# Performance work log

Measured on AMD Instinct MI355X. Metric: run time of the kernel, lower is better.

The kernel has to match this reference:

```python
import jax, jax.numpy as jnp
import numpy as np

NEG_INF = -1e30

def setup_inputs() -> dict:
    key = jax.random.key(0)
    k1, k2, k3 = jax.random.split(key, 3)
    B, H, S, D = 2, 16, 2048, 128
    q = jax.random.normal(k1, (B, H, S, D), dtype=jnp.float32)
    k = jax.random.normal(k2, (B, H, S, D), dtype=jnp.float32)
    v = jax.random.normal(k3, (B, H, S, D), dtype=jnp.float32)
    return {"q": q, "k": k, "v": v}

def reference(q, k, v):
    # F.scaled_dot_product_attention(q, k, v, is_causal=True), MATH backend:
    # full score matrix, causal mask (top-left aligned: j <= i), softmax, bmm.
    D = q.shape[-1]
    scale = 1.0 / jnp.sqrt(jnp.asarray(D, dtype=q.dtype))
    scores = jnp.einsum('bhqd,bhkd->bhqk', q, k) * scale  # [B,H,S,S]
    Sq, Sk = scores.shape[-2], scores.shape[-1]
    causal = jnp.arange(Sk)[None, :] <= jnp.arange(Sq)[:, None]  # [Sq,Sk]
    scores = jnp.where(causal[None, None], scores, NEG_INF)
    attn = jax.nn.softmax(scores, axis=-1)
    return jnp.einsum('bhqk,bhkd->bhqd', attn, v)
```

## Files before the change

kernel.cpp:

```cpp
#include <hip/hip_runtime.h>
#include <cstdint>
#include <cstddef>

typedef __attribute__((ext_vector_type(8))) short short8;
typedef __attribute__((ext_vector_type(4))) float floatx4;
typedef __attribute__((ext_vector_type(2))) unsigned int uint2v;

namespace {
constexpr int kBH  = 32;
constexpr int kS   = 2048;
constexpr int kD   = 128;
constexpr int kBQ  = 64;
constexpr int kBK  = 32;
constexpr int kNQT = kS / kBQ;
constexpr int PST  = 72;
constexpr size_t kKVElems = (size_t)kBH * kS * kD;
}

__device__ __forceinline__ unsigned short f32_bf16(float f) {
    union { float f; unsigned u; } c; c.f = f;
    unsigned u = c.u;
    u += 0x7FFFu + ((u >> 16) & 1u);
    return (unsigned short)(u >> 16);
}

__device__ __forceinline__ unsigned cvt_pk_bf16(float lo, float hi) {
    unsigned r;
    asm("v_cvt_pk_bf16_f32 %0, %1, %2" : "=v"(r) : "v"(lo), "v"(hi));
    return r;
}

__device__ __forceinline__ unsigned pack_bf16x2(float lo, float hi) {
    return cvt_pk_bf16(lo, hi);
}

__device__ __forceinline__ float fast_exp2(float x) {
#if __has_builtin(__builtin_amdgcn_exp2f)
    return __builtin_amdgcn_exp2f(x);
#else
    return __expf(x * 0.6931471805599453f);
#endif
}

__device__ __forceinline__ void gl_lds16(const void* g, void* l) {
    __builtin_amdgcn_global_load_lds(
        (const __attribute__((address_space(1))) unsigned int*)g,
        (__attribute__((address_space(3))) unsigned int*)l, 16, 0, 0);
}

__global__ __launch_bounds__(256)
void prepass(const float* __restrict__ K, const float* __restrict__ V,
             unsigned short* __restrict__ Kb, unsigned short* __restrict__ Vt) {
    const int b = (int)blockIdx.x;
    const int t = (int)threadIdx.x;
    if (b < 4096) {
        const size_t i0 = ((size_t)b * 256 + t) * 8;
        floatx4 a = *(const floatx4*)(K + i0);
        floatx4 c = *(const floatx4*)(K + i0 + 4);
        union { unsigned u[4]; short8 v; } pk;
        pk.u[0] = cvt_pk_bf16(a[0], a[1]);
        pk.u[1] = cvt_pk_bf16(a[2], a[3]);
        pk.u[2] = cvt_pk_bf16(c[0], c[1]);
        pk.u[3] = cvt_pk_bf16(c[2], c[3]);
        *(short8*)(Kb + i0) = pk.v;
    } else {
        __shared__ float ldsT[64][68];
        const int vb = b - 4096;
        const int bh = vb >> 6;
        const int rem = vb & 63;
        const int s0 = (rem >> 1) * 64;
        const int d0 = (rem & 1) * 64;
        const float* vbase = V + ((size_t)bh * kS + s0) * kD + d0;
        const int sr = t >> 4, c4 = (t & 15) * 4;
#pragma unroll
        for (int p = 0; p < 4; ++p) {
            const int s = p * 16 + sr;
            *(floatx4*)&ldsT[s][c4] = *(const floatx4*)(vbase + (size_t)s * kD + c4);
        }
        __syncthreads();
        const int dr = t >> 2, sc = (t & 3) * 16;
        union { unsigned u[8]; short8 v[2]; } pk;
#pragma unroll
        for (int j = 0; j < 8; ++j)
            pk.u[j] = cvt_pk_bf16(ldsT[sc + 2 * j][dr], ldsT[sc + 2 * j + 1][dr]);
        unsigned short* out = Vt + ((size_t)(bh * kD + d0 + dr)) * kS + s0 + sc;
        *(short8*)out = pk.v[0];
        *(short8*)(out + 8) = pk.v[1];
    }
}


__global__ __launch_bounds__(256, 4)
void fa_fwd_ws(const float* __restrict__ Qg, const unsigned short* __restrict__ Kb,
               const unsigned short* __restrict__ Vt, float* __restrict__ Og) {
    const int id = (int)blockIdx.x;
    const int s  = id >> 8;
    const int j  = id & 255;
    const int bh = (j & 7) * 4 + ((j >> 3) & 3);
    const int a  = j >> 5;
    const int qt = (s == 0) ? a : (s == 1) ? (31 - a) : (s == 2) ? (8 + a) : (23 - a);

    const int t    = (int)threadIdx.x;
    const int wave = t >> 6;
    const int lane = t & 63;
    const int quad = lane >> 4;
    const int l16  = lane & 15;
    const int rowq_base = qt * 64 + wave * 16 + l16;
    const int prm_lo = ((quad & 1) << 7) + (l16 << 2);
    const int prm_hi = prm_lo + 64;
    const bool hi = lane >= 32;

    __shared__ __align__(16) unsigned short kT0[kBK * 128];
    __shared__ __align__(16) unsigned short kT1[kBK * 128];
    __shared__ __align__(16) unsigned short vT0[kD * kBK];
    __shared__ __align__(16) unsigned short vT1[kD * kBK];

    const float scale = 0.12751744459649126f;

    short8  qf[4];
    floatx4 oacc[8];
    float   lsum = 0.f;
#pragma unroll
    for (int i = 0; i < 8; ++i) oacc[i] = (floatx4){0, 0, 0, 0};

    {
        const float* qp = Qg + ((size_t)bh * kS + rowq_base) * kD;
#pragma unroll
        for (int ks = 0; ks < 4; ++ks) {
            const int d0 = ks * 32 + quad * 8;
            floatx4 a0 = *(const floatx4*)(qp + d0);
            floatx4 a1 = *(const floatx4*)(qp + d0 + 4);
            union { unsigned u[4]; short8 v; } pa;
            pa.u[0] = cvt_pk_bf16(a0[0] * scale, a0[1] * scale);
            pa.u[1] = cvt_pk_bf16(a0[2] * scale, a0[3] * scale);
            pa.u[2] = cvt_pk_bf16(a1[0] * scale, a1[1] * scale);
            pa.u[3] = cvt_pk_bf16(a1[2] * scale, a1[3] * scale);
            qf[ks] = pa.v;
        }
    }

    const unsigned short* kBase = Kb + (size_t)bh * kS * kD;
    const unsigned short* vBase = Vt + (size_t)bh * kD * kS;

    auto stage = [&](int kt, unsigned short* kDst, unsigned short* vDst) {
        const int kj0 = kt * kBK;
#pragma unroll
        for (int i = 0; i < 2; ++i) {
            const int rbase = wave * 8 + i * 4;
            const int row = rbase + (lane >> 4);
            const int cg  = (lane & 15) ^ (row & 15);
            gl_lds16(kBase + ((size_t)(kj0 + row)) * kD + cg * 8,
                     &kDst[rbase * 128]);
        }
#pragma unroll
        for (int i = 0; i < 2; ++i) {
            const int dbase = wave * 32 + i * 16;
            const int d  = dbase + (lane >> 2);
            const int cg = (lane & 3) ^ ((d >> 1) & 3);
            gl_lds16(vBase + (size_t)d * kS + kj0 + cg * 8,
                     &vDst[dbase * kBK]);
        }
    };

    auto tile_step = [&](const unsigned short* kT, const unsigned short* vT,
                         bool doMask, int rq) {
        floatx4 sacc[2];
        __builtin_amdgcn_s_setprio(1);
#pragma unroll
        for (int nt = 0; nt < 2; ++nt) {
            floatx4 acc = (floatx4){0.f, 0.f, 0.f, 0.f};
#pragma unroll
            for (int ks = 0; ks < 4; ++ks) {
                short8 kf = *(const short8*)&kT[(nt * 16 + l16) * 128 + (((ks * 4 + quad) ^ l16) << 3)];
                acc = __builtin_amdgcn_mfma_f32_16x16x32_bf16(kf, qf[ks], acc, 0, 0, 0);
            }
            sacc[nt] = acc;
        }
        __builtin_amdgcn_s_setprio(0);

        float ls = 0.f;
#pragma unroll
        for (int nt = 0; nt < 2; ++nt)
#pragma unroll
            for (int r = 0; r < 4; ++r) {
                float e = fast_exp2(sacc[nt][r]);
                if (doMask && (nt * 16 + quad * 4 + r > rq)) e = 0.f;
                sacc[nt][r] = e;
                ls += e;
            }
        lsum += ls;

        unsigned pk0a = cvt_pk_bf16(sacc[0][0], sacc[0][1]);
        unsigned pk0b = cvt_pk_bf16(sacc[0][2], sacc[0][3]);
        unsigned pk1a = cvt_pk_bf16(sacc[1][0], sacc[1][1]);
        unsigned pk1b = cvt_pk_bf16(sacc[1][2], sacc[1][3]);
        int e0 = __builtin_amdgcn_ds_bpermute(prm_lo, (int)pk0a);
        int e1 = __builtin_amdgcn_ds_bpermute(prm_lo, (int)pk0b);
        int e2 = __builtin_amdgcn_ds_bpermute(prm_hi, (int)pk0a);
        int e3 = __builtin_amdgcn_ds_bpermute(prm_hi, (int)pk0b);
        int o0 = __builtin_amdgcn_ds_bpermute(prm_lo, (int)pk1a);
        int o1 = __builtin_amdgcn_ds_bpermute(prm_lo, (int)pk1b);
        int o2 = __builtin_amdgcn_ds_bpermute(prm_hi, (int)pk1a);
        int o3 = __builtin_amdgcn_ds_bpermute(prm_hi, (int)pk1b);
        union { unsigned u[4]; short8 v; } pf;
        pf.u[0] = hi ? (unsigned)o0 : (unsigned)e0;
        pf.u[1] = hi ? (unsigned)o1 : (unsigned)e1;
        pf.u[2] = hi ? (unsigned)o2 : (unsigned)e2;
        pf.u[3] = hi ? (unsigned)o3 : (unsigned)e3;

        __builtin_amdgcn_s_setprio(1);
#pragma unroll
        for (int nd = 0; nd < 8; ++nd) {
            short8 vf = *(const short8*)&vT[(nd * 16 + l16) * kBK + ((quad ^ ((l16 >> 1) & 3)) << 3)];
            oacc[nd] = __builtin_amdgcn_mfma_f32_16x16x32_bf16(pf.v, vf, oacc[nd], 0, 0, 0);
        }
        __builtin_amdgcn_s_setprio(0);
    };

    const int last = 2 * qt + 1;
    stage(0, kT0, vT0);
    __syncthreads();

    int kt = 0;
    for (;;) {
        if (kt < last) stage(kt + 1, kT1, vT1);
        tile_step(kT0, vT0, kt >= 2 * qt, rowq_base - kt * kBK);
        __syncthreads();
        if (kt == last) break;
        ++kt;
        if (kt < last) stage(kt + 1, kT0, vT0);
        tile_step(kT1, vT1, kt >= 2 * qt, rowq_base - kt * kBK);
        __syncthreads();
        if (kt == last) break;
        ++kt;
    }

    float rs = lsum;
    rs += __shfl_xor(rs, 16, 64);
    rs += __shfl_xor(rs, 32, 64);
    float inv[4];
#pragma unroll
    for (int r = 0; r < 4; ++r)
        inv[r] = 1.0f / __shfl(rs, quad * 4 + r, 64);
    float* ob = Og + ((size_t)bh * kS + qt * 64 + wave * 16 + quad * 4) * kD;
#pragma unroll
    for (int nd = 0; nd < 8; ++nd)
#pragma unroll
        for (int r = 0; r < 4; ++r)
            ob[(size_t)r * kD + nd * 16 + l16] = oacc[nd][r] * inv[r];
}

namespace {
constexpr int kBKf = 64;
constexpr int KSTf = 136;
constexpr int VSTf = 72;
}

struct TileStateF {
    short8  qf[4];
    floatx4 oacc[8];
    float   lsum[4];
};

__device__ __forceinline__ void tile_step_f(
    TileStateF& ts, const unsigned short* kT, const unsigned short* vT,
    unsigned short* pw, int l16, int quad, int rowl, bool doMask)
{
    floatx4 sacc[4];
    __builtin_amdgcn_s_setprio(1);
#pragma unroll
    for (int nt = 0; nt < 4; ++nt) {
        floatx4 acc = (floatx4){0.f, 0.f, 0.f, 0.f};
#pragma unroll
        for (int ks = 0; ks < 4; ++ks) {
            short8 kf = *(const short8*)&kT[(nt * 16 + l16) * KSTf + ks * 32 + quad * 8];
            acc = __builtin_amdgcn_mfma_f32_16x16x32_bf16(ts.qf[ks], kf, acc, 0, 0, 0);
        }
        sacc[nt] = acc;
    }
    __builtin_amdgcn_s_setprio(0);
    if (doMask) {
#pragma unroll
        for (int nt = 0; nt < 4; ++nt) {
            const int col = nt * 16 + l16;
#pragma unroll
            for (int r = 0; r < 4; ++r)
                if (col > rowl + r) sacc[nt][r] = -1e30f;
        }
    }
#pragma unroll
    for (int nt = 0; nt < 4; ++nt)
#pragma unroll
        for (int r = 0; r < 4; ++r)
            sacc[nt][r] = fast_exp2(sacc[nt][r]);
#pragma unroll
    for (int r = 0; r < 4; ++r)
        ts.lsum[r] += (sacc[0][r] + sacc[1][r]) + (sacc[2][r] + sacc[3][r]);
#pragma unroll
    for (int r = 0; r < 4; ++r) {
#pragma unroll
        for (int np = 0; np < 2; ++np) {
            const unsigned u = cvt_pk_bf16(sacc[np * 2][r], sacc[np * 2 + 1][r]);
            pw[(quad * 4 + r) * PST + (np * 2) * 16 + l16]     = (unsigned short)u;
            pw[(quad * 4 + r) * PST + (np * 2 + 1) * 16 + l16] = (unsigned short)(u >> 16);
        }
    }
    short8 pf[2];
#pragma unroll
    for (int ks = 0; ks < 2; ++ks)
        pf[ks] = *(const short8*)&pw[l16 * PST + ks * 32 + quad * 8];
    __builtin_amdgcn_s_setprio(1);
#pragma unroll
    for (int nd = 0; nd < 8; ++nd) {
        floatx4 acc = ts.oacc[nd];
#pragma unroll
        for (int ks = 0; ks < 2; ++ks) {
            short8 vf = *(const short8*)&vT[(nd * 16 + l16) * VSTf + ks * 32 + quad * 8];
            acc = __builtin_amdgcn_mfma_f32_16x16x32_bf16(pf[ks], vf, acc, 0, 0, 0);
        }
        ts.oacc[nd] = acc;
    }
    __builtin_amdgcn_s_setprio(0);
}

__global__ __launch_bounds__(256, 2)
void fa_fwd_fallback(const float* __restrict__ Qg, const float* __restrict__ Kg,
                     const float* __restrict__ Vg, float* __restrict__ Og) {
    const int id = (int)blockIdx.x;
    const int qA = id >> 5;
    const int qB = kNQT - 1 - qA;
    const int bh = id & (kBH - 1);
    const int t    = (int)threadIdx.x;
    const int wave = t >> 6;
    const int lane = t & 63;
    const int quad = lane >> 4;
    const int l16  = lane & 15;
    const int rowl = wave * 16 + quad * 4;

    __shared__ __align__(16) unsigned short kT[2][kBKf * KSTf];
    __shared__ __align__(16) unsigned short vT[2][kD * VSTf];
    __shared__ __align__(16) unsigned short pT[4 * 16 * PST];
    unsigned short* pw = &pT[wave * 16 * PST];

    const float scale = 0.12751744459649126f;

    TileStateF A, B;
#pragma unroll
    for (int i = 0; i < 8; ++i) { A.oacc[i] = (floatx4){0,0,0,0}; B.oacc[i] = (floatx4){0,0,0,0}; }
#pragma unroll
    for (int r = 0; r < 4; ++r) { A.lsum[r] = 0.f; B.lsum[r] = 0.f; }
    {
        const float* qpA = Qg + ((size_t)bh * kS + qA * kBQ + wave * 16 + l16) * kD;
        const float* qpB = Qg + ((size_t)bh * kS + qB * kBQ + wave * 16 + l16) * kD;
#pragma unroll
        for (int ks = 0; ks < 4; ++ks) {
            const int d0 = ks * 32 + quad * 8;
            floatx4 a0 = *(const floatx4*)(qpA + d0);
            floatx4 a1 = *(const floatx4*)(qpA + d0 + 4);
            floatx4 b0 = *(const floatx4*)(qpB + d0);
            floatx4 b1 = *(const floatx4*)(qpB + d0 + 4);
            union { unsigned u[4]; short8 v; } pa, pb;
            pa.u[0] = cvt_pk_bf16(a0[0] * scale, a0[1] * scale);
            pa.u[1] = cvt_pk_bf16(a0[2] * scale, a0[3] * scale);
            pa.u[2] = cvt_pk_bf16(a1[0] * scale, a1[1] * scale);
            pa.u[3] = cvt_pk_bf16(a1[2] * scale, a1[3] * scale);
            pb.u[0] = cvt_pk_bf16(b0[0] * scale, b0[1] * scale);
            pb.u[1] = cvt_pk_bf16(b0[2] * scale, b0[3] * scale);
            pb.u[2] = cvt_pk_bf16(b1[0] * scale, b1[1] * scale);
            pb.u[3] = cvt_pk_bf16(b1[2] * scale, b1[3] * scale);
            A.qf[ks] = pa.v;
            B.qf[ks] = pb.v;
        }
    }

    const int kRow8 = t >> 5;
    const int kCol4 = t & 31;
    const int vD    = t & 127;
    const int vR2   = t >> 7;
    const float* kBaseH = Kg + (size_t)bh * kS * kD;
    const float* vBaseH = Vg + (size_t)bh * kS * kD;
    floatx4 kpre[8];
    float   vpreL[16], vpreH[16];

    auto issue_kv_loads = [&](int kt) {
        const float* kb = kBaseH + (size_t)(kt * kBKf) * kD;
        const float* vb = vBaseH + (size_t)(kt * kBKf) * kD;
#pragma unroll
        for (int p = 0; p < 8; ++p)
            kpre[p] = *(const floatx4*)(kb + (size_t)(p * 8 + kRow8) * kD + kCol4 * 4);
#pragma unroll
        for (int p = 0; p < 16; ++p) {
            const int j = p * 2 + vR2;
            vpreL[p] = vb[(size_t)(2 * j) * kD + vD];
            vpreH[p] = vb[(size_t)(2 * j + 1) * kD + vD];
        }
    };
    auto store_kv = [&](int buf) {
#pragma unroll
        for (int p = 0; p < 8; ++p) {
            union { unsigned u[2]; uint2v v; } w;
            w.u[0] = cvt_pk_bf16(kpre[p][0], kpre[p][1]);
            w.u[1] = cvt_pk_bf16(kpre[p][2], kpre[p][3]);
            *(uint2v*)&kT[buf][(p * 8 + kRow8) * KSTf + kCol4 * 4] = w.v;
        }
#pragma unroll
        for (int p = 0; p < 16; ++p) {
            const int j = p * 2 + vR2;
            *(unsigned*)&vT[buf][vD * VSTf + 2 * j] = pack_bf16x2(vpreL[p], vpreH[p]);
        }
    };

    const int last = qB;
    issue_kv_loads(0);
    store_kv(0);
    __syncthreads();
    for (int kt = 0; kt <= last; ++kt) {
        const int buf = kt & 1;
        if (kt < last) issue_kv_loads(kt + 1);
        if (kt <= qA) tile_step_f(A, kT[buf], vT[buf], pw, l16, quad, rowl, kt == qA);
        tile_step_f(B, kT[buf], vT[buf], pw, l16, quad, rowl, kt == last);
        if (kt < last) {
            store_kv(buf ^ 1);
            __syncthreads();
        }
    }
#pragma unroll
    for (int tile = 0; tile < 2; ++tile) {
        TileStateF& ts = tile ? B : A;
        const int qt = tile ? qB : qA;
        float ls[4];
#pragma unroll
        for (int r = 0; r < 4; ++r) ls[r] = ts.lsum[r];
#pragma unroll
        for (int off = 1; off < 16; off <<= 1)
#pragma unroll
            for (int r = 0; r < 4; ++r)
                ls[r] += __shfl_xor(ls[r], off, 64);
        float inv[4];
#pragma unroll
        for (int r = 0; r < 4; ++r) inv[r] = 1.0f / ls[r];
        float* ob = Og + ((size_t)bh * kS + qt * kBQ + wave * 16 + quad * 4) * kD;
#pragma unroll
        for (int nd = 0; nd < 8; ++nd)
#pragma unroll
            for (int r = 0; r < 4; ++r)
                ob[(size_t)r * kD + nd * 16 + l16] = ts.oacc[nd][r] * inv[r];
    }
}

extern "C" void kernel_launch(void* const* d_in, const int* in_sizes, int n_in,
                              void* d_out, int out_size, void* d_ws, size_t ws_size,
                              hipStream_t stream) {
    (void)in_sizes; (void)n_in; (void)out_size;
    const float* q = (const float*)d_in[0];
    const float* k = (const float*)d_in[1];
    const float* v = (const float*)d_in[2];
    float* o = (float*)d_out;
    const size_t need = 2 * kKVElems * sizeof(unsigned short);
    if (ws_size >= need) {
        unsigned short* Kb = (unsigned short*)d_ws;
        unsigned short* Vt = Kb + kKVElems;
        prepass<<<dim3(4096 + 2048), 256, 0, stream>>>(k, v, Kb, Vt);
        fa_fwd_ws<<<dim3(kNQT * kBH), 256, 0, stream>>>(q, Kb, Vt, o);
    } else {
        fa_fwd_fallback<<<dim3((kNQT / 2) * kBH), 256, 0, stream>>>(q, k, v, o);
    }
}
```

Before: 186.5 us.

## Pair complementary causal q-tiles per 512-thread block sharing K/V tiles

```diff
diff --git a/kernel.cpp b/kernel.cpp
--- a/kernel.cpp
+++ b/kernel.cpp
@@ -11,17 +11,10 @@
 constexpr int kS   = 2048;
 constexpr int kD   = 128;
 constexpr int kBQ  = 64;
-constexpr int kBK  = 32;
+constexpr int kBK  = 64;
 constexpr int kNQT = kS / kBQ;
 constexpr int PST  = 72;
 constexpr size_t kKVElems = (size_t)kBH * kS * kD;
-}
-
-__device__ __forceinline__ unsigned short f32_bf16(float f) {
-    union { float f; unsigned u; } c; c.f = f;
-    unsigned u = c.u;
-    u += 0x7FFFu + ((u >> 16) & 1u);
-    return (unsigned short)(u >> 16);
 }
 
 __device__ __forceinline__ unsigned cvt_pk_bf16(float lo, float hi) {
@@ -40,12 +33,6 @@
 #else
     return __expf(x * 0.6931471805599453f);
 #endif
-}
-
-__device__ __forceinline__ void gl_lds16(const void* g, void* l) {
-    __builtin_amdgcn_global_load_lds(
-        (const __attribute__((address_space(1))) unsigned int*)g,
-        (__attribute__((address_space(3))) unsigned int*)l, 16, 0, 0);
 }
 
 __global__ __launch_bounds__(256)
@@ -89,31 +76,47 @@
     }
 }
 
-
-__global__ __launch_bounds__(256, 4)
+__device__ __forceinline__ short8 p_gather(unsigned pe0, unsigned pe1,
+                                           unsigned po0, unsigned po1,
+                                           int lane, int prm_lo, int prm_hi) {
+    int ce0 = __builtin_amdgcn_ds_bpermute(prm_lo, (int)pe0);
+    int ce1 = __builtin_amdgcn_ds_bpermute(prm_lo, (int)pe1);
+    int ce2 = __builtin_amdgcn_ds_bpermute(prm_hi, (int)pe0);
+    int ce3 = __builtin_amdgcn_ds_bpermute(prm_hi, (int)pe1);
+    int co0 = __builtin_amdgcn_ds_bpermute(prm_lo, (int)po0);
+    int co1 = __builtin_amdgcn_ds_bpermute(prm_lo, (int)po1);
+    int co2 = __builtin_amdgcn_ds_bpermute(prm_hi, (int)po0);
+    int co3 = __builtin_amdgcn_ds_bpermute(prm_hi, (int)po1);
+    const bool hi = lane >= 32;
+    union { unsigned u[4]; short8 v; } r;
+    r.u[0] = hi ? (unsigned)co0 : (unsigned)ce0;
+    r.u[1] = hi ? (unsigned)co1 : (unsigned)ce1;
+    r.u[2] = hi ? (unsigned)co2 : (unsigned)ce2;
+    r.u[3] = hi ? (unsigned)co3 : (unsigned)ce3;
+    return r.v;
+}
+
+__global__ __launch_bounds__(512, 4)
 void fa_fwd_ws(const float* __restrict__ Qg, const unsigned short* __restrict__ Kb,
                const unsigned short* __restrict__ Vt, float* __restrict__ Og) {
     const int id = (int)blockIdx.x;
-    const int s  = id >> 8;
-    const int j  = id & 255;
-    const int bh = (j & 7) * 4 + ((j >> 3) & 3);
-    const int a  = j >> 5;
-    const int qt = (s == 0) ? a : (s == 1) ? (31 - a) : (s == 2) ? (8 + a) : (23 - a);
-
+    const int qA = id >> 5;
+    const int qB = kNQT - 1 - qA;
+    const int bh = (id & 7) * 4 + ((id >> 3) & 3);
     const int t    = (int)threadIdx.x;
     const int wave = t >> 6;
+    const int g    = wave >> 2;
+    const int wsub = wave & 3;
     const int lane = t & 63;
     const int quad = lane >> 4;
     const int l16  = lane & 15;
-    const int rowq_base = qt * 64 + wave * 16 + l16;
-    const int prm_lo = ((quad & 1) << 7) + (l16 << 2);
+    const int qt   = g ? qB : qA;
+    const int rowq = wsub * 16 + l16;
+    const int prm_lo = (((lane >> 4) & 1) << 7) + (l16 << 2);
     const int prm_hi = prm_lo + 64;
-    const bool hi = lane >= 32;
-
-    __shared__ __align__(16) unsigned short kT0[kBK * 128];
-    __shared__ __align__(16) unsigned short kT1[kBK * 128];
-    __shared__ __align__(16) unsigned short vT0[kD * kBK];
-    __shared__ __align__(16) unsigned short vT1[kD * kBK];
+
+    __shared__ __align__(16) unsigned short kT[kBK * 128];
+    __shared__ __align__(16) unsigned short vT[kD * 64];
 
     const float scale = 0.12751744459649126f;
 
@@ -124,7 +127,7 @@
     for (int i = 0; i < 8; ++i) oacc[i] = (floatx4){0, 0, 0, 0};
 
     {
-        const float* qp = Qg + ((size_t)bh * kS + rowq_base) * kD;
+        const float* qp = Qg + ((size_t)bh * kS + qt * kBQ + wsub * 16 + l16) * kD;
 #pragma unroll
         for (int ks = 0; ks < 4; ++ks) {
             const int d0 = ks * 32 + quad * 8;
@@ -142,32 +145,41 @@
     const unsigned short* kBase = Kb + (size_t)bh * kS * kD;
     const unsigned short* vBase = Vt + (size_t)bh * kD * kS;
 
-    auto stage = [&](int kt, unsigned short* kDst, unsigned short* vDst) {
+    short8 stK[2], stV[2];
+    const int krow0 = wave * 8 + (lane >> 4);
+    const int kcg   = (lane & 15);
+    const int vd0   = wave * 16 + (lane >> 3);
+    const int vcg   = (lane & 7);
+
+    auto issue = [&](int kt) {
         const int kj0 = kt * kBK;
 #pragma unroll
         for (int i = 0; i < 2; ++i) {
-            const int rbase = wave * 8 + i * 4;
-            const int row = rbase + (lane >> 4);
-            const int cg  = (lane & 15) ^ (row & 15);
-            gl_lds16(kBase + ((size_t)(kj0 + row)) * kD + cg * 8,
-                     &kDst[rbase * 128]);
+            const int row = krow0 + i * 4;
+            const int cg  = kcg ^ (row & 15);
+            stK[i] = *(const short8*)(kBase + ((size_t)(kj0 + row)) * kD + cg * 8);
         }
 #pragma unroll
         for (int i = 0; i < 2; ++i) {
-            const int dbase = wave * 32 + i * 16;
-            const int d  = dbase + (lane >> 2);
-            const int cg = (lane & 3) ^ ((d >> 1) & 3);
-            gl_lds16(vBase + (size_t)d * kS + kj0 + cg * 8,
-                     &vDst[dbase * kBK]);
+            const int d  = vd0 + i * 8;
+            const int cg = vcg ^ (d & 7);
+            stV[i] = *(const short8*)(vBase + (size_t)d * kS + kj0 + cg * 8);
         }
     };
-
-    auto tile_step = [&](const unsigned short* kT, const unsigned short* vT,
-                         bool doMask, int rq) {
-        floatx4 sacc[2];
+    auto write_lds = [&]() {
+#pragma unroll
+        for (int i = 0; i < 2; ++i)
+            *(short8*)&kT[(wave * 8 + i * 4) * 128 + lane * 8] = stK[i];
+#pragma unroll
+        for (int i = 0; i < 2; ++i)
+            *(short8*)&vT[(wave * 16 + i * 8) * 64 + lane * 8] = stV[i];
+    };
+
+    auto tile_step = [&](bool doMask) {
+        floatx4 sacc[4];
         __builtin_amdgcn_s_setprio(1);
 #pragma unroll
-        for (int nt = 0; nt < 2; ++nt) {
+        for (int nt = 0; nt < 4; ++nt) {
             floatx4 acc = (floatx4){0.f, 0.f, 0.f, 0.f};
 #pragma unroll
             for (int ks = 0; ks < 4; ++ks) {
@@ -180,59 +192,57 @@
 
         float ls = 0.f;
 #pragma unroll
-        for (int nt = 0; nt < 2; ++nt)
+        for (int nt = 0; nt < 4; ++nt)
 #pragma unroll
             for (int r = 0; r < 4; ++r) {
                 float e = fast_exp2(sacc[nt][r]);
-                if (doMask && (nt * 16 + quad * 4 + r > rq)) e = 0.f;
+                if (doMask && (nt * 16 + quad * 4 + r > rowq)) e = 0.f;
                 sacc[nt][r] = e;
                 ls += e;
             }
         lsum += ls;
 
-        unsigned pk0a = cvt_pk_bf16(sacc[0][0], sacc[0][1]);
-        unsigned pk0b = cvt_pk_bf16(sacc[0][2], sacc[0][3]);
-        unsigned pk1a = cvt_pk_bf16(sacc[1][0], sacc[1][1]);
-        unsigned pk1b = cvt_pk_bf16(sacc[1][2], sacc[1][3]);
-        int e0 = __builtin_amdgcn_ds_bpermute(prm_lo, (int)pk0a);
-        int e1 = __builtin_amdgcn_ds_bpermute(prm_lo, (int)pk0b);
-        int e2 = __builtin_amdgcn_ds_bpermute(prm_hi, (int)pk0a);
-        int e3 = __builtin_amdgcn_ds_bpermute(prm_hi, (int)pk0b);
-        int o0 = __builtin_amdgcn_ds_bpermute(prm_lo, (int)pk1a);
-        int o1 = __builtin_amdgcn_ds_bpermute(prm_lo, (int)pk1b);
-        int o2 = __builtin_amdgcn_ds_bpermute(prm_hi, (int)pk1a);
-        int o3 = __builtin_amdgcn_ds_bpermute(prm_hi, (int)pk1b);
-        union { unsigned u[4]; short8 v; } pf;
-        pf.u[0] = hi ? (unsigned)o0 : (unsigned)e0;
-        pf.u[1] = hi ? (unsigned)o1 : (unsigned)e1;
-        pf.u[2] = hi ? (unsigned)o2 : (unsigned)e2;
-        pf.u[3] = hi ? (unsigned)o3 : (unsigned)e3;
+        unsigned pk[4][2];
+#pragma unroll
+        for (int nt = 0; nt < 4; ++nt) {
+            pk[nt][0] = cvt_pk_bf16(sacc[nt][0], sacc[nt][1]);
+            pk[nt][1] = cvt_pk_bf16(sacc[nt][2], sacc[nt][3]);
+        }
+        short8 pf[2];
+        pf[0] = p_gather(pk[0][0], pk[0][1], pk[1][0], pk[1][1], lane, prm_lo, prm_hi);
+        pf[1] = p_gather(pk[2][0], pk[2][1], pk[3][0], pk[3][1], lane, prm_lo, prm_hi);
 
         __builtin_amdgcn_s_setprio(1);
 #pragma unroll
         for (int nd = 0; nd < 8; ++nd) {
-            short8 vf = *(const short8*)&vT[(nd * 16 + l16) * kBK + ((quad ^ ((l16 >> 1) & 3)) << 3)];
-            oacc[nd] = __builtin_amdgcn_mfma_f32_16x16x32_bf16(pf.v, vf, oacc[nd], 0, 0, 0);
+            floatx4 acc = oacc[nd];
+#pragma unroll
+            for (int ks = 0; ks < 2; ++ks) {
+                short8 vf = *(const short8*)&vT[(nd * 16 + l16) * 64 + ((((ks * 4 + quad)) ^ (l16 & 7)) << 3)];
+                acc = __builtin_amdgcn_mfma_f32_16x16x32_bf16(pf[ks], vf, acc, 0, 0, 0);
+            }
+            oacc[nd] = acc;
         }
         __builtin_amdgcn_s_setprio(0);
     };
 
-    const int last = 2 * qt + 1;
-    stage(0, kT0, vT0);
-    __syncthreads();
-
-    int kt = 0;
-    for (;;) {
-        if (kt < last) stage(kt + 1, kT1, vT1);
-        tile_step(kT0, vT0, kt >= 2 * qt, rowq_base - kt * kBK);
-        __syncthreads();
-        if (kt == last) break;
-        ++kt;
-        if (kt < last) stage(kt + 1, kT0, vT0);
-        tile_step(kT1, vT1, kt >= 2 * qt, rowq_base - kt * kBK);
-        __syncthreads();
-        if (kt == last) break;
-        ++kt;
+    issue(0);
+    write_lds();
+    asm volatile("s_waitcnt lgkmcnt(0)" ::: "memory");
+    __builtin_amdgcn_s_barrier();
+    __builtin_amdgcn_sched_barrier(0);
+
+    for (int kt = 0;; ++kt) {
+        if (kt < qB) issue(kt + 1);
+        if (kt <= qt) tile_step(kt == qt);
+        if (kt == qB) break;
+        asm volatile("" ::: "memory");
+        __builtin_amdgcn_s_barrier();
+        __builtin_amdgcn_sched_barrier(0);
+        write_lds();
+        asm volatile("s_waitcnt lgkmcnt(0)" ::: "memory");
+        __builtin_amdgcn_s_barrier();
+        __builtin_amdgcn_sched_barrier(0);
     }
 
     float rs = lsum;
@@ -242,7 +252,7 @@
 #pragma unroll
     for (int r = 0; r < 4; ++r)
         inv[r] = 1.0f / __shfl(rs, quad * 4 + r, 64);
-    float* ob = Og + ((size_t)bh * kS + qt * 64 + wave * 16 + quad * 4) * kD;
+    float* ob = Og + ((size_t)bh * kS + qt * kBQ + wsub * 16 + quad * 4) * kD;
 #pragma unroll
     for (int nd = 0; nd < 8; ++nd)
 #pragma unroll
@@ -461,7 +471,7 @@
         unsigned short* Kb = (unsigned short*)d_ws;
         unsigned short* Vt = Kb + kKVElems;
         prepass<<<dim3(4096 + 2048), 256, 0, stream>>>(k, v, Kb, Vt);
-        fa_fwd_ws<<<dim3(kNQT * kBH), 256, 0, stream>>>(q, Kb, Vt, o);
+        fa_fwd_ws<<<dim3((kNQT / 2) * kBH), 512, 0, stream>>>(q, Kb, Vt, o);
     } else {
         fa_fwd_fallback<<<dim3((kNQT / 2) * kBH), 256, 0, stream>>>(q, k, v, o);
     }
```

Measured after the change: 181.3 us. -2.8%, faster.
